# Optimization experiments

Hardware: AMD Instinct MI355X
Metric: run time of the kernel (lower is better)

## Reference

```python
import jax, jax.numpy as jnp
import numpy as np

D = 16          # input_dim (no augmentations)
HID = 256       # hidden_dim
WIN = 64        # window_size
LEN = 1000      # len_noise
INTU = 50       # len_interval_u
B = 512
PAIRS = D * (D - 1) // 2      # 120 depth-2 Lyndon pairs
LOGSIG = D + PAIRS            # 136 logsignature channels


def _static_schedule():
    """Replicates compute_multilevel_logsignature's index logic on static times."""
    tb = np.linspace(0.0, 1.0, LEN)
    tu = tb[::INTU]
    tt = np.linspace(0.0, 1.0, WIN)
    u_indices = np.searchsorted(tb, tu, side='right') - 1
    t_indices = np.searchsorted(tb, tt[1:], side='right') - 1
    u_idx_for_t = np.searchsorted(tu, tt[1:], side='right') - 1
    start_idx = u_indices[np.maximum(u_idx_for_t, 0)]
    # build u_logsigrnn times and the per-step last_h update mask
    qt, last = [], -1
    for iu in u_idx_for_t:
        iu = max(int(iu), 0)
        if iu != last:
            qt.append(tu[iu]); last = iu
    qt.append(tt[-1])
    upd = np.zeros(WIN, dtype=bool)
    for i, t in enumerate(tt):
        if qt and t >= qt[0]:
            qt.pop(0); upd[i] = True
    return tb, t_indices, start_idx, upd


def setup_inputs() -> dict:
    key = jax.random.key(0)
    ks = jax.random.split(key, 6)
    def lin(k, fo, fi):  # kaiming-style fan_in init
        return jax.random.normal(k, (fo, fi), jnp.float32) * np.float32(np.sqrt(2.0 / fi))
    return {
        "z": jax.random.normal(ks[0], (B, LEN, D), jnp.float32),
        "W1": lin(ks[1], HID, HID + LOGSIG), "b1": jnp.zeros((HID,), jnp.float32),
        "W2": lin(ks[2], HID, HID),          "b2": jnp.zeros((HID,), jnp.float32),
        "W3": lin(ks[3], HID, HID),          "b3": jnp.zeros((HID,), jnp.float32),
        "W_lin": lin(ks[4], HID, HID),
    }


def reference(z, W1, b1, W2, b2, W3, b3, W_lin):
    tb, t_idx, s_idx, upd = _static_schedule()
    # Brownian path: z[:,0]=0, z[:,1:] *= sqrt(dt), cumsum
    dt_sqrt = jnp.sqrt(jnp.asarray(np.diff(tb), jnp.float32))          # [LEN-1]
    z = jnp.concatenate([jnp.zeros_like(z[:, :1]), z[:, 1:] * dt_sqrt[None, :, None]], axis=1)
    X = jnp.cumsum(z, axis=1)                                           # [B,LEN,D]
    # depth-2 logsignature with basepoint=0: level1 = X[end]; level2 = Levy area
    iu, ju = np.triu_indices(D, 1)
    Xp, dX = X[:, :-1], X[:, 1:] - X[:, :-1]
    pair = Xp[..., iu] * dX[..., ju] - Xp[..., ju] * dX[..., iu]        # [B,LEN-1,PAIRS]
    C = jnp.concatenate([jnp.zeros_like(pair[:, :1]), jnp.cumsum(pair, axis=1)], axis=1)
    lvl1 = X[:, t_idx]
    levy = 0.5 * (C[:, t_idx] - C[:, s_idx])
    logsig = jnp.concatenate([lvl1, levy], axis=-1)
    logsig = jnp.concatenate([jnp.zeros_like(logsig[:, :1]), logsig], axis=1)  # prepend zeros
    seq = jnp.moveaxis(logsig, 1, 0)

    def mlp(v):  # FeedForwardNN([hid,hid]) + Tanh
        v = jax.nn.relu(v @ W1.T + b1)
        v = jax.nn.relu(v @ W2.T + b2)
        return jnp.tanh(v @ W3.T + b3)

    def step(last_h, xs):
        ls, u = xs
        h = mlp(jnp.concatenate([last_h, ls], axis=-1))
        new_last = jnp.where(u, h, last_h)
        return new_last, h @ W_lin.T

    h0 = jnp.zeros((z.shape[0], HID), z.dtype)  # init_fixed=True
    _, ys = jax.lax.scan(step, h0, (seq, jnp.asarray(upd)))
    return jnp.moveaxis(ys, 0, 1)
```

## Files before the change

### kernel.cpp

```cpp
#include <hip/hip_runtime.h>
#include <hip/hip_bf16.h>
#include <cmath>
#include <cstring>

#define B_SZ   512
#define SLEN   1000
#define DD     16
#define HID    256
#define WIN    64
#define PAIRS  120
#define LSIG   136
#define NWIN   20
#define MAXST  21
#define K1P    416
#define W1FN   (13 * 16 * 64 * 8)
#define WFN    (8 * 16 * 64 * 8)
#define PSTEP  21

using short8 = __attribute__((ext_vector_type(8))) short;
using half8  = __attribute__((ext_vector_type(8))) _Float16;
using f32x4  = __attribute__((ext_vector_type(4))) float;

struct SchedArgs { short snapk[SLEN - 1]; };
struct CombArgs  { unsigned char winofm[WIN]; unsigned char zl[WIN]; };
struct ChainArgs { int nsteps; unsigned char kU[32]; };
struct FuseArgs  { unsigned char sidx[WIN]; };

__device__ __forceinline__ unsigned short f2h(float x) {
  _Float16 h = (_Float16)x;
  return __builtin_bit_cast(unsigned short, h);
}
__device__ __forceinline__ float ftanh(float x) {
  float t = fminf(fmaxf(2.f * x, -30.f), 30.f);
  float e = __expf(t);
  return (e - 1.f) / (e + 1.f);
}

__global__ __launch_bounds__(128) void prep_kernel(
    const float* __restrict__ z,
    const float* __restrict__ W1, const float* __restrict__ W2,
    const float* __restrict__ W3, const float* __restrict__ Wl,
    float* __restrict__ logsig, float* __restrict__ dxwin,
    unsigned short* __restrict__ W1f, unsigned short* __restrict__ W2f,
    unsigned short* __restrict__ W3f, unsigned short* __restrict__ Wlf,
    SchedArgs A)
{
  const int w = blockIdx.x, b = blockIdx.y, tid = threadIdx.x;
  if (w >= NWIN) {
    const int slot = ((w - NWIN) * B_SZ + b) * 128 + tid;
    for (int e = slot; e < W1FN + 3 * WFN; e += 3 * B_SZ * 128) {
      if (e < W1FN) {
        int f = e;
        int j = f & 7, l15 = (f >> 3) & 15, lq = (f >> 7) & 3, nsub = (f >> 9) & 15, kk = f >> 13;
        int row = nsub * 16 + l15, col = kk * 32 + lq * 8 + j;
        float v = (col < HID + LSIG) ? W1[(size_t)row * (HID + LSIG) + col] : 0.f;
        W1f[f] = f2h(v);
      } else {
        int e2 = e - W1FN;
        int which = e2 >> 16, f = e2 & 65535;
        int j = f & 7, l15 = (f >> 3) & 15, lq = (f >> 7) & 3, nsub = (f >> 9) & 15, kk = (f >> 13) & 7;
        int row = nsub * 16 + l15, col = kk * 32 + lq * 8 + j;
        const float* src = which == 0 ? W2 : which == 1 ? W3 : Wl;
        unsigned short* dst = which == 0 ? W2f : which == 1 ? W3f : Wlf;
        dst[f] = f2h(src[(size_t)row * HID + col]);
      }
    }
    return;
  }
  __shared__ float zs[50][16];
  const int ns = (w == NWIN - 1) ? 49 : 50;
  const float* src = z + ((size_t)b * SLEN + 50 * w + 1) * DD;
  const double s999 = 1.0 / (double)(SLEN - 1);
  for (int c = tid; c < ns * 4; c += 128) {
    float4 v = ((const float4*)src)[c];
    int t = 50 * w + (c >> 2);
    double a = (t + 1 == SLEN - 1) ? 1.0 : (double)(t + 1) * s999;
    float s = sqrtf((float)(a - (double)t * s999));
    v.x *= s; v.y *= s; v.z *= s; v.w *= s;
    ((float4*)&zs[0][0])[c] = v;
  }
  int pi = 0, pj = 0;
  if (tid < PAIRS) { int rem = tid, i = 0; while (rem >= DD - 1 - i) { rem -= DD - 1 - i; ++i; } pi = i; pj = i + 1 + rem; }
  __syncthreads();
  float Yi = 0.f, Yj = 0.f, LL = 0.f, Yd = 0.f;
  const int base_t = 50 * w;
  for (int u = 0; u < ns; ++u) {
    const float di = zs[u][pi], dj = zs[u][pj];
    LL = fmaf(Yi, dj, LL); LL = fmaf(-Yj, di, LL);
    Yi += di; Yj += dj;
    if (tid < DD) Yd += zs[u][tid];
    const int m = A.snapk[base_t + u];
    if (m) {
      float* dst = logsig + ((size_t)b * WIN + m) * LSIG;
      if (tid < DD)    dst[tid]      = Yd;
      if (tid < PAIRS) dst[DD + tid] = LL;
    }
  }
  if (tid < DD) dxwin[((size_t)b * NWIN + w) * DD + tid] = Yd;
}

__global__ __launch_bounds__(128) void comb_kernel(
    float* __restrict__ logsig, const float* __restrict__ dxwin, CombArgs A)
{
  const int m = blockIdx.x, b = blockIdx.y, tid = threadIdx.x;
  float* row = logsig + ((size_t)b * WIN + m) * LSIG;
  if (m == 0) {
    if (tid < LSIG) row[tid] = 0.f;
    if (tid + 128 < LSIG) row[tid + 128] = 0.f;
    return;
  }
  __shared__ float Xs[DD], Yt[DD];
  const int w = A.winofm[m];
  if (tid < DD) {
    float acc = 0.f;
    for (int ww = 0; ww < w; ++ww) acc += dxwin[((size_t)b * NWIN + ww) * DD + tid];
    float y = row[tid];
    Xs[tid] = acc; Yt[tid] = y;
    row[tid] = acc + y;
  }
  __syncthreads();
  if (tid < PAIRS) {
    int rem = tid, i = 0; while (rem >= DD - 1 - i) { rem -= DD - 1 - i; ++i; }
    const int pi = i, pj = i + 1 + rem;
    float ll = row[DD + tid];
    row[DD + tid] = A.zl[m] ? 0.f : 0.5f * (ll + Xs[pi] * Yt[pj] - Xs[pj] * Yt[pi]);
  }
}

__global__ __launch_bounds__(256) void psig_kernel(
    const float* __restrict__ logsig, const unsigned short* __restrict__ W1f,
    const float* __restrict__ b1, float* __restrict__ partial, ChainArgs A)
{
  __shared__ __align__(16) unsigned short As[5 * 4 * 16 * 8];
  const int g = blockIdx.x, m = blockIdx.y, tid = threadIdx.x;
  const int lane = tid & 63, w = tid >> 6;
  const int l15 = lane & 15, lq = lane >> 4;
  const int k = A.kU[m];
  for (int idx = tid; idx < 16 * 160; idx += 256) {
    int row = idx / 160, c = idx - row * 160;
    float v = (c < LSIG) ? logsig[(((size_t)(g * 16 + row)) * WIN + k) * LSIG + c] : 0.f;
    As[(((c >> 5) * 4 + ((c >> 3) & 3)) * 16 + row) * 8 + (c & 7)] = f2h(v);
  }
  __syncthreads();
  f32x4 acc[4] = {{0.f,0.f,0.f,0.f},{0.f,0.f,0.f,0.f},{0.f,0.f,0.f,0.f},{0.f,0.f,0.f,0.f}};
#pragma unroll
  for (int kt = 0; kt < 5; ++kt) {
    half8 af = *(const half8*)&As[((kt * 4 + lq) * 16 + l15) * 8];
#pragma unroll
    for (int t = 0; t < 4; ++t) {
      half8 bf = *(const half8*)(W1f + ((size_t)((8 + kt) * 16 + w * 4 + t) * 64 + lane) * 8);
      acc[t] = __builtin_amdgcn_mfma_f32_16x16x32_f16(af, bf, acc[t], 0, 0, 0);
    }
  }
#pragma unroll
  for (int t = 0; t < 4; ++t) {
    int col = w * 64 + t * 16 + l15;
    float bb = b1[col];
    f32x4 r = acc[t];
    r[0] += bb; r[1] += bb; r[2] += bb; r[3] += bb;
    *(f32x4*)&partial[(((size_t)g * PSTEP + m) * HID + col) * 16 + lq * 4] = r;
  }
}

__global__ __attribute__((amdgpu_flat_work_group_size(512, 512)))
__attribute__((amdgpu_waves_per_eu(2, 2)))
void chain_kernel(
    const float* __restrict__ partial,
    const unsigned short* __restrict__ W1f, const unsigned short* __restrict__ W2f,
    const unsigned short* __restrict__ W3f,
    const float* __restrict__ b2, const float* __restrict__ b3,
    unsigned short* __restrict__ statesb, ChainArgs A)
{
  __shared__ __align__(16) unsigned short A0s[32 * 16 * 8];
  __shared__ __align__(16) unsigned short A1s[32 * 16 * 8];
  __shared__ __align__(16) unsigned short A2s[32 * 16 * 8];
  const int tid = threadIdx.x, g = blockIdx.x;
  const int lane = tid & 63, w = tid >> 6;
  const int l15 = lane & 15, lq = lane >> 4;

  for (int c = tid; c < 32 * 16 * 8; c += 512) A0s[c] = 0;
  for (int c = tid; c < 16 * HID; c += 512) {
    int r = c >> 8, col = c & 255;
    statesb[((size_t)(g * 16 + r) * MAXST + 0) * HID + col] = 0;
  }

  half8 W1r[16], W2r[16], W3r[16];
#pragma unroll
  for (int kk = 0; kk < 8; ++kk)
#pragma unroll
    for (int nt = 0; nt < 2; ++nt) {
      W1r[kk * 2 + nt] = *(const half8*)(W1f + ((size_t)(kk * 16 + w * 2 + nt) * 64 + lane) * 8);
      W2r[kk * 2 + nt] = *(const half8*)(W2f + ((size_t)(kk * 16 + w * 2 + nt) * 64 + lane) * 8);
      W3r[kk * 2 + nt] = *(const half8*)(W3f + ((size_t)(kk * 16 + w * 2 + nt) * 64 + lane) * 8);
    }

  float bias2[2], bias3[2];
#pragma unroll
  for (int nt = 0; nt < 2; ++nt) {
    int col = (w * 2 + nt) * 16 + l15;
    bias2[nt] = b2[col]; bias3[nt] = b3[col];
  }

  const float* pbase = partial + ((size_t)g * PSTEP) * HID * 16;
  int poff[2];
#pragma unroll
  for (int nt = 0; nt < 2; ++nt) {
    int col = w * 32 + nt * 16 + l15;
    poff[nt] = col * 16 + lq * 4;
  }
  f32x4 pf[2];
  pf[0] = *(const f32x4*)(pbase + poff[0]);
  pf[1] = *(const f32x4*)(pbase + poff[1]);

  unsigned short hv[2][4];
  __syncthreads();

  for (int m = 0; m < A.nsteps; ++m) {
    if (m > 0) {
#pragma unroll
      for (int nt = 0; nt < 2; ++nt)
#pragma unroll
        for (int r4 = 0; r4 < 4; ++r4) {
          int row = lq * 4 + r4, col = w * 32 + nt * 16 + l15;
          statesb[((size_t)(g * 16 + row) * MAXST + m) * HID + col] = hv[nt][r4];
        }
    }
    {
      f32x4 acc[2][2];
      acc[0][0] = pf[0]; acc[0][1] = pf[1];
      acc[1][0] = (f32x4){0.f,0.f,0.f,0.f}; acc[1][1] = (f32x4){0.f,0.f,0.f,0.f};
      if (m + 1 < A.nsteps) {
        const float* pp = pbase + (size_t)(m + 1) * HID * 16;
        pf[0] = *(const f32x4*)(pp + poff[0]);
        pf[1] = *(const f32x4*)(pp + poff[1]);
      }
#pragma unroll
      for (int kk = 0; kk < 8; ++kk) {
        half8 af = *(const half8*)&A0s[((kk * 4 + lq) * 16 + l15) * 8];
        acc[kk & 1][0] = __builtin_amdgcn_mfma_f32_16x16x32_f16(af, W1r[kk * 2    ], acc[kk & 1][0], 0, 0, 0);
        acc[kk & 1][1] = __builtin_amdgcn_mfma_f32_16x16x32_f16(af, W1r[kk * 2 + 1], acc[kk & 1][1], 0, 0, 0);
      }
#pragma unroll
      for (int nt = 0; nt < 2; ++nt) {
        f32x4 s = acc[0][nt] + acc[1][nt];
        int col = w * 32 + nt * 16 + l15;
        int base = ((col >> 3) * 16) * 8 + (col & 7);
#pragma unroll
        for (int r4 = 0; r4 < 4; ++r4)
          A1s[base + (lq * 4 + r4) * 8] = f2h(fmaxf(s[r4], 0.f));
      }
    }
    __syncthreads();
    {
      f32x4 acc[2][2] = {{{0.f,0.f,0.f,0.f},{0.f,0.f,0.f,0.f}},{{0.f,0.f,0.f,0.f},{0.f,0.f,0.f,0.f}}};
#pragma unroll
      for (int kk = 0; kk < 8; ++kk) {
        half8 af = *(const half8*)&A1s[((kk * 4 + lq) * 16 + l15) * 8];
        acc[kk & 1][0] = __builtin_amdgcn_mfma_f32_16x16x32_f16(af, W2r[kk * 2    ], acc[kk & 1][0], 0, 0, 0);
        acc[kk & 1][1] = __builtin_amdgcn_mfma_f32_16x16x32_f16(af, W2r[kk * 2 + 1], acc[kk & 1][1], 0, 0, 0);
      }
#pragma unroll
      for (int nt = 0; nt < 2; ++nt) {
        f32x4 s = acc[0][nt] + acc[1][nt];
        int col = w * 32 + nt * 16 + l15;
        int base = ((col >> 3) * 16) * 8 + (col & 7);
#pragma unroll
        for (int r4 = 0; r4 < 4; ++r4)
          A2s[base + (lq * 4 + r4) * 8] = f2h(fmaxf(s[r4] + bias2[nt], 0.f));
      }
    }
    __syncthreads();
    {
      f32x4 acc[2][2] = {{{0.f,0.f,0.f,0.f},{0.f,0.f,0.f,0.f}},{{0.f,0.f,0.f,0.f},{0.f,0.f,0.f,0.f}}};
#pragma unroll
      for (int kk = 0; kk < 8; ++kk) {
        half8 af = *(const half8*)&A2s[((kk * 4 + lq) * 16 + l15) * 8];
        acc[kk & 1][0] = __builtin_amdgcn_mfma_f32_16x16x32_f16(af, W3r[kk * 2    ], acc[kk & 1][0], 0, 0, 0);
        acc[kk & 1][1] = __builtin_amdgcn_mfma_f32_16x16x32_f16(af, W3r[kk * 2 + 1], acc[kk & 1][1], 0, 0, 0);
      }
#pragma unroll
      for (int nt = 0; nt < 2; ++nt) {
        f32x4 s = acc[0][nt] + acc[1][nt];
        int col = w * 32 + nt * 16 + l15;
        int base = ((col >> 3) * 16) * 8 + (col & 7);
#pragma unroll
        for (int r4 = 0; r4 < 4; ++r4) {
          float tv = ftanh(s[r4] + bias3[nt]);
          unsigned short hvv = f2h(tv);
          hv[nt][r4] = hvv;
          A0s[base + (lq * 4 + r4) * 8] = hvv;
        }
      }
    }
    __syncthreads();
  }
  {
    const int m = A.nsteps;
#pragma unroll
    for (int nt = 0; nt < 2; ++nt)
#pragma unroll
      for (int r4 = 0; r4 < 4; ++r4) {
        int row = lq * 4 + r4, col = w * 32 + nt * 16 + l15;
        statesb[((size_t)(g * 16 + row) * MAXST + m) * HID + col] = hv[nt][r4];
      }
  }
}

__global__ __launch_bounds__(256, 1) void fused_kernel(
    const unsigned short* __restrict__ statesb, const float* __restrict__ logsig,
    const unsigned short* __restrict__ W1f, const unsigned short* __restrict__ W2f,
    const unsigned short* __restrict__ W3f, const unsigned short* __restrict__ Wlf,
    const float* __restrict__ b1, const float* __restrict__ b2, const float* __restrict__ b3,
    float* __restrict__ out, FuseArgs F)
{
  __shared__ __align__(16) unsigned short act1[32 * 128 * 8];
  __shared__ __align__(16) unsigned short act2[32 * 128 * 8];
  __shared__ __align__(16) unsigned short atile[2][4 * 128 * 8];
  const int tid = threadIdx.x, band = blockIdx.x;
  const int lane = tid & 63, w = tid >> 6;
  const int l15 = lane & 15, lq = lane >> 4;

  float bias1[4], bias2[4], bias3[4];
#pragma unroll
  for (int t = 0; t < 4; ++t) {
    int col = w * 64 + t * 16 + l15;
    bias1[t] = b1[col]; bias2[t] = b2[col]; bias3[t] = b3[col];
  }

  f32x4 acc[8][4];
#pragma unroll
  for (int a = 0; a < 8; ++a)
#pragma unroll
    for (int t = 0; t < 4; ++t) acc[a][t] = (f32x4){0.f, 0.f, 0.f, 0.f};

  short8 pk[2];
  auto loadA = [&](int kk, short8* p) {
#pragma unroll
    for (int i = 0; i < 2; ++i) {
      int c = tid + 256 * i;
      int r = c >> 2, cc = (c & 3) * 8;
      int col = kk * 32 + cc;
      int bA = band * 2 + (r >> 6), ks = r & 63;
      if (col < HID) {
        p[i] = *(const short8*)(statesb + ((size_t)bA * MAXST + F.sidx[ks]) * HID + col);
      } else {
        const float* sp = logsig + ((size_t)bA * WIN + ks) * LSIG + (col - HID);
        float4 v0 = ((const float4*)sp)[0];
        float4 v1 = ((const float4*)sp)[1];
        short8 q;
        q[0] = (short)f2h(v0.x); q[1] = (short)f2h(v0.y); q[2] = (short)f2h(v0.z); q[3] = (short)f2h(v0.w);
        q[4] = (short)f2h(v1.x); q[5] = (short)f2h(v1.y); q[6] = (short)f2h(v1.z); q[7] = (short)f2h(v1.w);
        p[i] = q;
      }
    }
  };
  loadA(0, pk);
  for (int kk = 0; kk < 13; ++kk) {
    unsigned short* buf = atile[kk & 1];
#pragma unroll
    for (int i = 0; i < 2; ++i) {
      int c = tid + 256 * i;
      int r = c >> 2, ch = c & 3;
      *(short8*)&buf[(ch * 128 + r) * 8] = pk[i];
    }
    __syncthreads();
    if (kk + 1 < 13) loadA(kk + 1, pk);
    half8 bfr[4];
#pragma unroll
    for (int t = 0; t < 4; ++t)
      bfr[t] = *(const half8*)(W1f + ((size_t)(kk * 16 + w * 4 + t) * 64 + lane) * 8);
#pragma unroll
    for (int a = 0; a < 8; ++a) {
      half8 af = *(const half8*)&buf[(lq * 128 + a * 16 + l15) * 8];
#pragma unroll
      for (int t = 0; t < 4; ++t)
        acc[a][t] = __builtin_amdgcn_mfma_f32_16x16x32_f16(af, bfr[t], acc[a][t], 0, 0, 0);
    }
    __syncthreads();
  }
#pragma unroll
  for (int a = 0; a < 8; ++a)
#pragma unroll
    for (int t = 0; t < 4; ++t) {
      int col = w * 64 + t * 16 + l15;
      int base = ((col >> 3) * 128) * 8 + (col & 7);
#pragma unroll
      for (int r4 = 0; r4 < 4; ++r4) {
        int row = a * 16 + lq * 4 + r4;
        act1[base + row * 8] = f2h(fmaxf(acc[a][t][r4] + bias1[t], 0.f));
      }
    }
  __syncthreads();

  auto layer = [&](const unsigned short* inb, const unsigned short* Wf) {
#pragma unroll
    for (int a = 0; a < 8; ++a)
#pragma unroll
      for (int t = 0; t < 4; ++t) acc[a][t] = (f32x4){0.f, 0.f, 0.f, 0.f};
    for (int kk = 0; kk < 8; ++kk) {
      half8 bfr[4];
#pragma unroll
      for (int t = 0; t < 4; ++t)
        bfr[t] = *(const half8*)(Wf + ((size_t)(kk * 16 + w * 4 + t) * 64 + lane) * 8);
#pragma unroll
      for (int a = 0; a < 8; ++a) {
        half8 af = *(const half8*)&inb[((kk * 4 + lq) * 128 + a * 16 + l15) * 8];
#pragma unroll
        for (int t = 0; t < 4; ++t)
          acc[a][t] = __builtin_amdgcn_mfma_f32_16x16x32_f16(af, bfr[t], acc[a][t], 0, 0, 0);
      }
    }
  };

  layer(act1, W2f);
#pragma unroll
  for (int a = 0; a < 8; ++a)
#pragma unroll
    for (int t = 0; t < 4; ++t) {
      int col = w * 64 + t * 16 + l15;
      int base = ((col >> 3) * 128) * 8 + (col & 7);
#pragma unroll
      for (int r4 = 0; r4 < 4; ++r4) {
        int row = a * 16 + lq * 4 + r4;
        act2[base + row * 8] = f2h(fmaxf(acc[a][t][r4] + bias2[t], 0.f));
      }
    }
  __syncthreads();

  layer(act2, W3f);
#pragma unroll
  for (int a = 0; a < 8; ++a)
#pragma unroll
    for (int t = 0; t < 4; ++t) {
      int col = w * 64 + t * 16 + l15;
      int base = ((col >> 3) * 128) * 8 + (col & 7);
#pragma unroll
      for (int r4 = 0; r4 < 4; ++r4) {
        int row = a * 16 + lq * 4 + r4;
        act1[base + row * 8] = f2h(ftanh(acc[a][t][r4] + bias3[t]));
      }
    }
  __syncthreads();

  layer(act1, Wlf);
#pragma unroll
  for (int a = 0; a < 8; ++a)
#pragma unroll
    for (int t = 0; t < 4; ++t) {
      int col = w * 64 + t * 16 + l15;
#pragma unroll
      for (int r4 = 0; r4 < 4; ++r4) {
        int row = a * 16 + lq * 4 + r4;
        out[((size_t)(band * 128 + row)) * HID + col] = acc[a][t][r4];
      }
    }
}

static void build_sched(SchedArgs& P, CombArgs& CB, ChainArgs& CH, FuseArgs& FU) {
  double tb[SLEN], tt[WIN], tu[NWIN];
  const double s999 = 1.0 / (double)(SLEN - 1);
  const double s63  = 1.0 / (double)(WIN - 1);
  for (int i = 0; i < SLEN; ++i) tb[i] = (double)i * s999;
  tb[SLEN - 1] = 1.0;
  for (int k = 0; k < WIN; ++k) tt[k] = (double)k * s63;
  tt[WIN - 1] = 1.0;
  for (int j = 0; j < NWIN; ++j) tu[j] = tb[50 * j];

  int t_idx[WIN - 1], u_for_t[WIN - 1];
  for (int k = 1; k < WIN; ++k) {
    int ii = 0;
    for (int q = 0; q < SLEN; ++q) if (tb[q] <= tt[k]) ii = q;
    t_idx[k - 1] = ii;
    int jj = 0;
    for (int q = 0; q < NWIN; ++q) if (tu[q] <= tt[k]) jj = q;
    u_for_t[k - 1] = jj;
  }
  for (int t = 0; t < SLEN - 1; ++t) P.snapk[t] = 0;
  for (int m = 1; m < WIN; ++m) P.snapk[t_idx[m - 1] - 1] = (short)m;

  for (int m = 0; m < WIN; ++m) { CB.winofm[m] = 0; CB.zl[m] = 0; }
  for (int m = 1; m < WIN; ++m) {
    int p = t_idx[m - 1];
    CB.winofm[m] = (unsigned char)((p - 1) / 50);
    CB.zl[m] = (p % 50 == 0) ? 1 : 0;
  }

  double qt[32]; int nq = 0, last = -1;
  for (int m = 0; m < WIN - 1; ++m) {
    const int iu = u_for_t[m];
    if (iu != last) { qt[nq++] = tu[iu]; last = iu; }
  }
  qt[nq++] = tt[WIN - 1];
  int upd[WIN]; int qh = 0;
  for (int i = 0; i < WIN; ++i) {
    upd[i] = 0;
    if (qh < nq && tt[i] >= qt[qh]) { qh++; upd[i] = 1; }
  }
  int nU = 0;
  for (int k = 0; k < WIN; ++k) if (upd[k]) { if (nU < 32) CH.kU[nU] = (unsigned char)k; ++nU; }
  int cnt = 0;
  for (int k = 0; k < WIN; ++k) { FU.sidx[k] = (unsigned char)cnt; if (upd[k]) ++cnt; }
  CH.nsteps = FU.sidx[WIN - 1];
}

extern "C" void kernel_launch(void* const* d_in, const int* in_sizes, int n_in,
                              void* d_out, int out_size, void* d_ws, size_t ws_size,
                              hipStream_t stream) {
  const float* z  = (const float*)d_in[0];
  const float* W1 = (const float*)d_in[1];
  const float* b1 = (const float*)d_in[2];
  const float* W2 = (const float*)d_in[3];
  const float* b2 = (const float*)d_in[4];
  const float* W3 = (const float*)d_in[5];
  const float* b3 = (const float*)d_in[6];
  const float* Wl = (const float*)d_in[7];

  char* ws = (char*)d_ws;
  float* logsig = (float*)(ws);
  size_t o = (size_t)B_SZ * WIN * LSIG * 4;
  float* dxwin            = (float*)(ws + o); o += (size_t)B_SZ * NWIN * DD * 4;
  unsigned short* statesb = (unsigned short*)(ws + o); o += (size_t)B_SZ * MAXST * HID * 2;
  unsigned short* W1f     = (unsigned short*)(ws + o); o += (size_t)W1FN * 2;
  unsigned short* W2f     = (unsigned short*)(ws + o); o += (size_t)WFN * 2;
  unsigned short* W3f     = (unsigned short*)(ws + o); o += (size_t)WFN * 2;
  unsigned short* Wlf     = (unsigned short*)(ws + o); o += (size_t)WFN * 2;
  float* partial          = (float*)(ws + o); o += (size_t)32 * PSTEP * HID * 16 * 4;

  SchedArgs P; CombArgs CB; ChainArgs CH; FuseArgs FU;
  build_sched(P, CB, CH, FU);

  prep_kernel<<<dim3(NWIN + 3, B_SZ), 128, 0, stream>>>(
      z, W1, W2, W3, Wl, logsig, dxwin, W1f, W2f, W3f, Wlf, P);
  comb_kernel<<<dim3(WIN, B_SZ), 128, 0, stream>>>(logsig, dxwin, CB);
  psig_kernel<<<dim3(32, CH.nsteps), 256, 0, stream>>>(logsig, W1f, b1, partial, CH);
  chain_kernel<<<32, 512, 0, stream>>>(partial, W1f, W2f, W3f, b2, b3, statesb, CH);
  fused_kernel<<<256, 256, 0, stream>>>(statesb, logsig, W1f, W2f, W3f, Wlf,
                                        b1, b2, b3, (float*)d_out, FU);
}
```

Baseline: 248.5 us.

## Fuse logsig combine with partial W1 projection and transpose MFMA operands for vector stores

Merges the combine kernel and the logsignature-to-hidden projection kernel into one kernel. Each block handles 16 batch rows for one window step, finalises their logsignature rows and immediately runs the MFMA projection for update steps, which removes one launch and a logsig reload. All MFMA calls swap their A/B operands so each lane holds four consecutive columns. Activations, states and outputs can then be written with vectorised 4-wide stores and biases loaded as f32x4. The partial buffer layout changes to row-major per step to match, and one barrier in the fused layer-1 loop is dropped.

After: 230.5 us. 7.3% less time.

```diff
diff --git a/kernel.cpp b/kernel.cpp
--- a/kernel.cpp
+++ b/kernel.cpp
@@ -17,12 +17,13 @@
 #define WFN    (8 * 16 * 64 * 8)
 #define PSTEP  21
 
-using short8 = __attribute__((ext_vector_type(8))) short;
-using half8  = __attribute__((ext_vector_type(8))) _Float16;
-using f32x4  = __attribute__((ext_vector_type(4))) float;
+using short8  = __attribute__((ext_vector_type(8))) short;
+using short4v = __attribute__((ext_vector_type(4))) short;
+using half8   = __attribute__((ext_vector_type(8))) _Float16;
+using f32x4   = __attribute__((ext_vector_type(4))) float;
 
 struct SchedArgs { short snapk[SLEN - 1]; };
-struct CombArgs  { unsigned char winofm[WIN]; unsigned char zl[WIN]; };
+struct CombPArgs { unsigned char winofm[WIN]; unsigned char zl[WIN]; unsigned char sstep[WIN]; };
 struct ChainArgs { int nsteps; unsigned char kU[32]; };
 struct FuseArgs  { unsigned char sidx[WIN]; };
 
@@ -99,66 +100,60 @@
   if (tid < DD) dxwin[((size_t)b * NWIN + w) * DD + tid] = Yd;
 }
 
-__global__ __launch_bounds__(128) void comb_kernel(
-    float* __restrict__ logsig, const float* __restrict__ dxwin, CombArgs A)
+__global__ __launch_bounds__(256) void combp_kernel(
+    float* __restrict__ logsig, const float* __restrict__ dxwin,
+    const unsigned short* __restrict__ W1f, const float* __restrict__ b1,
+    float* __restrict__ partial, CombPArgs A)
 {
-  const int m = blockIdx.x, b = blockIdx.y, tid = threadIdx.x;
-  float* row = logsig + ((size_t)b * WIN + m) * LSIG;
-  if (m == 0) {
-    if (tid < LSIG) row[tid] = 0.f;
-    if (tid + 128 < LSIG) row[tid + 128] = 0.f;
-    return;
-  }
-  __shared__ float Xs[DD], Yt[DD];
-  const int w = A.winofm[m];
-  if (tid < DD) {
+  __shared__ float Xs[16][16], Yt[16][16];
+  __shared__ __align__(16) unsigned short As[20 * 16 * 8];
+  const int k = blockIdx.x, g = blockIdx.y, tid = threadIdx.x;
+  const int w = A.winofm[k], zl = A.zl[k], ss = A.sstep[k];
+  for (int c = tid; c < 3 * 16 * 8; c += 256) As[17 * 16 * 8 + c] = 0;
+  {
+    const int bi = tid >> 4, col = tid & 15;
+    const size_t b = (size_t)(g * 16 + bi);
     float acc = 0.f;
-    for (int ww = 0; ww < w; ++ww) acc += dxwin[((size_t)b * NWIN + ww) * DD + tid];
-    float y = row[tid];
-    Xs[tid] = acc; Yt[tid] = y;
-    row[tid] = acc + y;
-  }
-  __syncthreads();
-  if (tid < PAIRS) {
-    int rem = tid, i = 0; while (rem >= DD - 1 - i) { rem -= DD - 1 - i; ++i; }
+    for (int ww = 0; ww < w; ++ww) acc += dxwin[(b * NWIN + ww) * DD + col];
+    float y = (k == 0) ? 0.f : logsig[(b * WIN + k) * LSIG + col];
+    float fin = (k == 0) ? 0.f : acc + y;
+    Xs[bi][col] = acc; Yt[bi][col] = y;
+    logsig[(b * WIN + k) * LSIG + col] = fin;
+    As[((col >> 3) * 16 + bi) * 8 + (col & 7)] = f2h(fin);
+  }
+  __syncthreads();
+  for (int idx = tid; idx < 16 * PAIRS; idx += 256) {
+    const int bi = idx / PAIRS, p = idx - bi * PAIRS;
+    int rem = p, i = 0; while (rem >= DD - 1 - i) { rem -= DD - 1 - i; ++i; }
     const int pi = i, pj = i + 1 + rem;
-    float ll = row[DD + tid];
-    row[DD + tid] = A.zl[m] ? 0.f : 0.5f * (ll + Xs[pi] * Yt[pj] - Xs[pj] * Yt[pi]);
-  }
-}
-
-__global__ __launch_bounds__(256) void psig_kernel(
-    const float* __restrict__ logsig, const unsigned short* __restrict__ W1f,
-    const float* __restrict__ b1, float* __restrict__ partial, ChainArgs A)
-{
-  __shared__ __align__(16) unsigned short As[5 * 4 * 16 * 8];
-  const int g = blockIdx.x, m = blockIdx.y, tid = threadIdx.x;
-  const int lane = tid & 63, w = tid >> 6;
+    const size_t b = (size_t)(g * 16 + bi);
+    float ll = (k == 0) ? 0.f : logsig[(b * WIN + k) * LSIG + DD + p];
+    float fin = (k == 0 || zl) ? 0.f
+              : 0.5f * (ll + Xs[bi][pi] * Yt[bi][pj] - Xs[bi][pj] * Yt[bi][pi]);
+    logsig[(b * WIN + k) * LSIG + DD + p] = fin;
+    const int c = DD + p;
+    As[((c >> 3) * 16 + bi) * 8 + (c & 7)] = f2h(fin);
+  }
+  if (ss == 255) return;
+  __syncthreads();
+  const int lane = tid & 63, wv = tid >> 6;
   const int l15 = lane & 15, lq = lane >> 4;
-  const int k = A.kU[m];
-  for (int idx = tid; idx < 16 * 160; idx += 256) {
-    int row = idx / 160, c = idx - row * 160;
-    float v = (c < LSIG) ? logsig[(((size_t)(g * 16 + row)) * WIN + k) * LSIG + c] : 0.f;
-    As[(((c >> 5) * 4 + ((c >> 3) & 3)) * 16 + row) * 8 + (c & 7)] = f2h(v);
-  }
-  __syncthreads();
-  f32x4 acc[4] = {{0.f,0.f,0.f,0.f},{0.f,0.f,0.f,0.f},{0.f,0.f,0.f,0.f},{0.f,0.f,0.f,0.f}};
+  f32x4 acc4[4] = {{0,0,0,0},{0,0,0,0},{0,0,0,0},{0,0,0,0}};
 #pragma unroll
   for (int kt = 0; kt < 5; ++kt) {
     half8 af = *(const half8*)&As[((kt * 4 + lq) * 16 + l15) * 8];
 #pragma unroll
     for (int t = 0; t < 4; ++t) {
-      half8 bf = *(const half8*)(W1f + ((size_t)((8 + kt) * 16 + w * 4 + t) * 64 + lane) * 8);
-      acc[t] = __builtin_amdgcn_mfma_f32_16x16x32_f16(af, bf, acc[t], 0, 0, 0);
+      half8 bfW = *(const half8*)(W1f + ((size_t)((8 + kt) * 16 + wv * 4 + t) * 64 + lane) * 8);
+      acc4[t] = __builtin_amdgcn_mfma_f32_16x16x32_f16(bfW, af, acc4[t], 0, 0, 0);
     }
   }
 #pragma unroll
   for (int t = 0; t < 4; ++t) {
-    int col = w * 64 + t * 16 + l15;
-    float bb = b1[col];
-    f32x4 r = acc[t];
-    r[0] += bb; r[1] += bb; r[2] += bb; r[3] += bb;
-    *(f32x4*)&partial[(((size_t)g * PSTEP + m) * HID + col) * 16 + lq * 4] = r;
+    const int col0 = wv * 64 + t * 16 + lq * 4;
+    f32x4 bb = *(const f32x4*)(b1 + col0);
+    f32x4 r = acc4[t] + bb;
+    *(f32x4*)&partial[(((size_t)g * PSTEP + ss) * 16 + l15) * HID + col0] = r;
   }
 }
 
@@ -194,60 +189,54 @@
       W3r[kk * 2 + nt] = *(const half8*)(W3f + ((size_t)(kk * 16 + w * 2 + nt) * 64 + lane) * 8);
     }
 
-  float bias2[2], bias3[2];
+  int colb[2];
+  f32x4 bias2v[2], bias3v[2];
 #pragma unroll
   for (int nt = 0; nt < 2; ++nt) {
-    int col = (w * 2 + nt) * 16 + l15;
-    bias2[nt] = b2[col]; bias3[nt] = b3[col];
-  }
-
-  const float* pbase = partial + ((size_t)g * PSTEP) * HID * 16;
+    colb[nt] = w * 32 + nt * 16 + lq * 4;
+    bias2v[nt] = *(const f32x4*)(b2 + colb[nt]);
+    bias3v[nt] = *(const f32x4*)(b3 + colb[nt]);
+  }
+
+  const float* pbase = partial + (size_t)g * PSTEP * 16 * HID;
   int poff[2];
 #pragma unroll
-  for (int nt = 0; nt < 2; ++nt) {
-    int col = w * 32 + nt * 16 + l15;
-    poff[nt] = col * 16 + lq * 4;
-  }
+  for (int nt = 0; nt < 2; ++nt) poff[nt] = l15 * HID + colb[nt];
   f32x4 pf[2];
   pf[0] = *(const f32x4*)(pbase + poff[0]);
   pf[1] = *(const f32x4*)(pbase + poff[1]);
 
-  unsigned short hv[2][4];
+  short4v hv4[2];
   __syncthreads();
 
   for (int m = 0; m < A.nsteps; ++m) {
     if (m > 0) {
 #pragma unroll
       for (int nt = 0; nt < 2; ++nt)
-#pragma unroll
-        for (int r4 = 0; r4 < 4; ++r4) {
-          int row = lq * 4 + r4, col = w * 32 + nt * 16 + l15;
-          statesb[((size_t)(g * 16 + row) * MAXST + m) * HID + col] = hv[nt][r4];
-        }
+        *(short4v*)&statesb[((size_t)(g * 16 + l15) * MAXST + m) * HID + colb[nt]] = hv4[nt];
     }
     {
       f32x4 acc[2][2];
       acc[0][0] = pf[0]; acc[0][1] = pf[1];
       acc[1][0] = (f32x4){0.f,0.f,0.f,0.f}; acc[1][1] = (f32x4){0.f,0.f,0.f,0.f};
       if (m + 1 < A.nsteps) {
-        const float* pp = pbase + (size_t)(m + 1) * HID * 16;
+        const float* pp = pbase + (size_t)(m + 1) * 16 * HID;
         pf[0] = *(const f32x4*)(pp + poff[0]);
         pf[1] = *(const f32x4*)(pp + poff[1]);
       }
 #pragma unroll
       for (int kk = 0; kk < 8; ++kk) {
         half8 af = *(const half8*)&A0s[((kk * 4 + lq) * 16 + l15) * 8];
-        acc[kk & 1][0] = __builtin_amdgcn_mfma_f32_16x16x32_f16(af, W1r[kk * 2    ], acc[kk & 1][0], 0, 0, 0);
-        acc[kk & 1][1] = __builtin_amdgcn_mfma_f32_16x16x32_f16(af, W1r[kk * 2 + 1], acc[kk & 1][1], 0, 0, 0);
+        acc[kk & 1][0] = __builtin_amdgcn_mfma_f32_16x16x32_f16(W1r[kk * 2    ], af, acc[kk & 1][0], 0, 0, 0);
+        acc[kk & 1][1] = __builtin_amdgcn_mfma_f32_16x16x32_f16(W1r[kk * 2 + 1], af, acc[kk & 1][1], 0, 0, 0);
       }
 #pragma unroll
       for (int nt = 0; nt < 2; ++nt) {
         f32x4 s = acc[0][nt] + acc[1][nt];
-        int col = w * 32 + nt * 16 + l15;
-        int base = ((col >> 3) * 16) * 8 + (col & 7);
-#pragma unroll
-        for (int r4 = 0; r4 < 4; ++r4)
-          A1s[base + (lq * 4 + r4) * 8] = f2h(fmaxf(s[r4], 0.f));
+        short4v h4;
+#pragma unroll
+        for (int r4 = 0; r4 < 4; ++r4) h4[r4] = (short)f2h(fmaxf(s[r4], 0.f));
+        *(short4v*)&A1s[((colb[nt] >> 3) * 16 + l15) * 8 + (colb[nt] & 7)] = h4;
       }
     }
     __syncthreads();
@@ -256,17 +245,16 @@
 #pragma unroll
       for (int kk = 0; kk < 8; ++kk) {
         half8 af = *(const half8*)&A1s[((kk * 4 + lq) * 16 + l15) * 8];
-        acc[kk & 1][0] = __builtin_amdgcn_mfma_f32_16x16x32_f16(af, W2r[kk * 2    ], acc[kk & 1][0], 0, 0, 0);
-        acc[kk & 1][1] = __builtin_amdgcn_mfma_f32_16x16x32_f16(af, W2r[kk * 2 + 1], acc[kk & 1][1], 0, 0, 0);
+        acc[kk & 1][0] = __builtin_amdgcn_mfma_f32_16x16x32_f16(W2r[kk * 2    ], af, acc[kk & 1][0], 0, 0, 0);
+        acc[kk & 1][1] = __builtin_amdgcn_mfma_f32_16x16x32_f16(W2r[kk * 2 + 1], af, acc[kk & 1][1], 0, 0, 0);
       }
 #pragma unroll
       for (int nt = 0; nt < 2; ++nt) {
-        f32x4 s = acc[0][nt] + acc[1][nt];
-        int col = w * 32 + nt * 16 + l15;
-        int base = ((col >> 3) * 16) * 8 + (col & 7);
-#pragma unroll
-        for (int r4 = 0; r4 < 4; ++r4)
-          A2s[base + (lq * 4 + r4) * 8] = f2h(fmaxf(s[r4] + bias2[nt], 0.f));
+        f32x4 s = acc[0][nt] + acc[1][nt] + bias2v[nt];
+        short4v h4;
+#pragma unroll
+        for (int r4 = 0; r4 < 4; ++r4) h4[r4] = (short)f2h(fmaxf(s[r4], 0.f));
+        *(short4v*)&A2s[((colb[nt] >> 3) * 16 + l15) * 8 + (colb[nt] & 7)] = h4;
       }
     }
     __syncthreads();
@@ -275,21 +263,17 @@
 #pragma unroll
       for (int kk = 0; kk < 8; ++kk) {
         half8 af = *(const half8*)&A2s[((kk * 4 + lq) * 16 + l15) * 8];
-        acc[kk & 1][0] = __builtin_amdgcn_mfma_f32_16x16x32_f16(af, W3r[kk * 2    ], acc[kk & 1][0], 0, 0, 0);
-        acc[kk & 1][1] = __builtin_amdgcn_mfma_f32_16x16x32_f16(af, W3r[kk * 2 + 1], acc[kk & 1][1], 0, 0, 0);
+        acc[kk & 1][0] = __builtin_amdgcn_mfma_f32_16x16x32_f16(W3r[kk * 2    ], af, acc[kk & 1][0], 0, 0, 0);
+        acc[kk & 1][1] = __builtin_amdgcn_mfma_f32_16x16x32_f16(W3r[kk * 2 + 1], af, acc[kk & 1][1], 0, 0, 0);
       }
 #pragma unroll
       for (int nt = 0; nt < 2; ++nt) {
-        f32x4 s = acc[0][nt] + acc[1][nt];
-        int col = w * 32 + nt * 16 + l15;
-        int base = ((col >> 3) * 16) * 8 + (col & 7);
-#pragma unroll
-        for (int r4 = 0; r4 < 4; ++r4) {
-          float tv = ftanh(s[r4] + bias3[nt]);
-          unsigned short hvv = f2h(tv);
-          hv[nt][r4] = hvv;
-          A0s[base + (lq * 4 + r4) * 8] = hvv;
-        }
+        f32x4 s = acc[0][nt] + acc[1][nt] + bias3v[nt];
+        short4v h4;
+#pragma unroll
+        for (int r4 = 0; r4 < 4; ++r4) h4[r4] = (short)f2h(ftanh(s[r4]));
+        hv4[nt] = h4;
+        *(short4v*)&A0s[((colb[nt] >> 3) * 16 + l15) * 8 + (colb[nt] & 7)] = h4;
       }
     }
     __syncthreads();
@@ -298,11 +282,7 @@
     const int m = A.nsteps;
 #pragma unroll
     for (int nt = 0; nt < 2; ++nt)
-#pragma unroll
-      for (int r4 = 0; r4 < 4; ++r4) {
-        int row = lq * 4 + r4, col = w * 32 + nt * 16 + l15;
-        statesb[((size_t)(g * 16 + row) * MAXST + m) * HID + col] = hv[nt][r4];
-      }
+      *(short4v*)&statesb[((size_t)(g * 16 + l15) * MAXST + m) * HID + colb[nt]] = hv4[nt];
   }
 }
 
@@ -319,13 +299,6 @@
   const int tid = threadIdx.x, band = blockIdx.x;
   const int lane = tid & 63, w = tid >> 6;
   const int l15 = lane & 15, lq = lane >> 4;
-
-  float bias1[4], bias2[4], bias3[4];
-#pragma unroll
-  for (int t = 0; t < 4; ++t) {
-    int col = w * 64 + t * 16 + l15;
-    bias1[t] = b1[col]; bias2[t] = b2[col]; bias3[t] = b3[col];
-  }
 
   f32x4 acc[8][4];
 #pragma unroll
@@ -356,7 +329,7 @@
   };
   loadA(0, pk);
   for (int kk = 0; kk < 13; ++kk) {
-    unsigned short* buf = atile[kk & 1];
+    unsigned short* buf = &atile[kk & 1][0];
 #pragma unroll
     for (int i = 0; i < 2; ++i) {
       int c = tid + 256 * i;
@@ -374,22 +347,22 @@
       half8 af = *(const half8*)&buf[(lq * 128 + a * 16 + l15) * 8];
 #pragma unroll
       for (int t = 0; t < 4; ++t)
-        acc[a][t] = __builtin_amdgcn_mfma_f32_16x16x32_f16(af, bfr[t], acc[a][t], 0, 0, 0);
-    }
-    __syncthreads();
-  }
-#pragma unroll
-  for (int a = 0; a < 8; ++a)
-#pragma unroll
-    for (int t = 0; t < 4; ++t) {
-      int col = w * 64 + t * 16 + l15;
-      int base = ((col >> 3) * 128) * 8 + (col & 7);
-#pragma unroll
-      for (int r4 = 0; r4 < 4; ++r4) {
-        int row = a * 16 + lq * 4 + r4;
-        act1[base + row * 8] = f2h(fmaxf(acc[a][t][r4] + bias1[t], 0.f));
-      }
-    }
+        acc[a][t] = __builtin_amdgcn_mfma_f32_16x16x32_f16(bfr[t], af, acc[a][t], 0, 0, 0);
+    }
+  }
+#pragma unroll
+  for (int t = 0; t < 4; ++t) {
+    const int col0 = w * 64 + t * 16 + lq * 4;
+    f32x4 bb = *(const f32x4*)(b1 + col0);
+#pragma unroll
+    for (int a = 0; a < 8; ++a) {
+      const int row = a * 16 + l15;
+      short4v h4;
+#pragma unroll
+      for (int r4 = 0; r4 < 4; ++r4) h4[r4] = (short)f2h(fmaxf(acc[a][t][r4] + bb[r4], 0.f));
+      *(short4v*)&act1[((col0 >> 3) * 128 + row) * 8 + (col0 & 7)] = h4;
+    }
+  }
   __syncthreads();
 
   auto layer = [&](const unsigned short* inb, const unsigned short* Wf) {
@@ -407,56 +380,56 @@
         half8 af = *(const half8*)&inb[((kk * 4 + lq) * 128 + a * 16 + l15) * 8];
 #pragma unroll
         for (int t = 0; t < 4; ++t)
-          acc[a][t] = __builtin_amdgcn_mfma_f32_16x16x32_f16(af, bfr[t], acc[a][t], 0, 0, 0);
+          acc[a][t] = __builtin_amdgcn_mfma_f32_16x16x32_f16(bfr[t], af, acc[a][t], 0, 0, 0);
       }
     }
   };
 
   layer(act1, W2f);
 #pragma unroll
-  for (int a = 0; a < 8; ++a)
-#pragma unroll
-    for (int t = 0; t < 4; ++t) {
-      int col = w * 64 + t * 16 + l15;
-      int base = ((col >> 3) * 128) * 8 + (col & 7);
-#pragma unroll
-      for (int r4 = 0; r4 < 4; ++r4) {
-        int row = a * 16 + lq * 4 + r4;
-        act2[base + row * 8] = f2h(fmaxf(acc[a][t][r4] + bias2[t], 0.f));
-      }
-    }
+  for (int t = 0; t < 4; ++t) {
+    const int col0 = w * 64 + t * 16 + lq * 4;
+    f32x4 bb = *(const f32x4*)(b2 + col0);
+#pragma unroll
+    for (int a = 0; a < 8; ++a) {
+      const int row = a * 16 + l15;
+      short4v h4;
+#pragma unroll
+      for (int r4 = 0; r4 < 4; ++r4) h4[r4] = (short)f2h(fmaxf(acc[a][t][r4] + bb[r4], 0.f));
+      *(short4v*)&act2[((col0 >> 3) * 128 + row) * 8 + (col0 & 7)] = h4;
+    }
+  }
   __syncthreads();
 
   layer(act2, W3f);
 #pragma unroll
-  for (int a = 0; a < 8; ++a)
-#pragma unroll
-    for (int t = 0; t < 4; ++t) {
-      int col = w * 64 + t * 16 + l15;
-      int base = ((col >> 3) * 128) * 8 + (col & 7);
-#pragma unroll
-      for (int r4 = 0; r4 < 4; ++r4) {
-        int row = a * 16 + lq * 4 + r4;
-        act1[base + row * 8] = f2h(ftanh(acc[a][t][r4] + bias3[t]));
-      }
-    }
+  for (int t = 0; t < 4; ++t) {
+    const int col0 = w * 64 + t * 16 + lq * 4;
+    f32x4 bb = *(const f32x4*)(b3 + col0);
+#pragma unroll
+    for (int a = 0; a < 8; ++a) {
+      const int row = a * 16 + l15;
+      short4v h4;
+#pragma unroll
+      for (int r4 = 0; r4 < 4; ++r4) h4[r4] = (short)f2h(ftanh(acc[a][t][r4] + bb[r4]));
+      *(short4v*)&act1[((col0 >> 3) * 128 + row) * 8 + (col0 & 7)] = h4;
+    }
+  }
   __syncthreads();
 
   layer(act1, Wlf);
 #pragma unroll
-  for (int a = 0; a < 8; ++a)
-#pragma unroll
-    for (int t = 0; t < 4; ++t) {
-      int col = w * 64 + t * 16 + l15;
-#pragma unroll
-      for (int r4 = 0; r4 < 4; ++r4) {
-        int row = a * 16 + lq * 4 + r4;
-        out[((size_t)(band * 128 + row)) * HID + col] = acc[a][t][r4];
-      }
-    }
-}
-
-static void build_sched(SchedArgs& P, CombArgs& CB, ChainArgs& CH, FuseArgs& FU) {
+  for (int t = 0; t < 4; ++t) {
+    const int col0 = w * 64 + t * 16 + lq * 4;
+#pragma unroll
+    for (int a = 0; a < 8; ++a) {
+      const int row = a * 16 + l15;
+      *(f32x4*)&out[((size_t)(band * 128 + row)) * HID + col0] = acc[a][t];
+    }
+  }
+}
+
+static void build_sched(SchedArgs& P, CombPArgs& CB, ChainArgs& CH, FuseArgs& FU) {
   double tb[SLEN], tt[WIN], tu[NWIN];
   const double s999 = 1.0 / (double)(SLEN - 1);
   const double s63  = 1.0 / (double)(WIN - 1);
@@ -478,7 +451,7 @@
   for (int t = 0; t < SLEN - 1; ++t) P.snapk[t] = 0;
   for (int m = 1; m < WIN; ++m) P.snapk[t_idx[m - 1] - 1] = (short)m;
 
-  for (int m = 0; m < WIN; ++m) { CB.winofm[m] = 0; CB.zl[m] = 0; }
+  for (int m = 0; m < WIN; ++m) { CB.winofm[m] = 0; CB.zl[m] = 0; CB.sstep[m] = 255; }
   for (int m = 1; m < WIN; ++m) {
     int p = t_idx[m - 1];
     CB.winofm[m] = (unsigned char)((p - 1) / 50);
@@ -501,6 +474,8 @@
   int cnt = 0;
   for (int k = 0; k < WIN; ++k) { FU.sidx[k] = (unsigned char)cnt; if (upd[k]) ++cnt; }
   CH.nsteps = FU.sidx[WIN - 1];
+  for (int s = 0; s < nU && s < 32; ++s)
+    if (s < PSTEP) CB.sstep[CH.kU[s]] = (unsigned char)s;
 }
 
 extern "C" void kernel_launch(void* const* d_in, const int* in_sizes, int n_in,
@@ -524,15 +499,14 @@
   unsigned short* W2f     = (unsigned short*)(ws + o); o += (size_t)WFN * 2;
   unsigned short* W3f     = (unsigned short*)(ws + o); o += (size_t)WFN * 2;
   unsigned short* Wlf     = (unsigned short*)(ws + o); o += (size_t)WFN * 2;
-  float* partial          = (float*)(ws + o); o += (size_t)32 * PSTEP * HID * 16 * 4;
-
-  SchedArgs P; CombArgs CB; ChainArgs CH; FuseArgs FU;
+  float* partial          = (float*)(ws + o); o += (size_t)32 * PSTEP * 16 * HID * 4;
+
+  SchedArgs P; CombPArgs CB; ChainArgs CH; FuseArgs FU;
   build_sched(P, CB, CH, FU);
 
   prep_kernel<<<dim3(NWIN + 3, B_SZ), 128, 0, stream>>>(
       z, W1, W2, W3, Wl, logsig, dxwin, W1f, W2f, W3f, Wlf, P);
-  comb_kernel<<<dim3(WIN, B_SZ), 128, 0, stream>>>(logsig, dxwin, CB);
-  psig_kernel<<<dim3(32, CH.nsteps), 256, 0, stream>>>(logsig, W1f, b1, partial, CH);
+  combp_kernel<<<dim3(WIN, 32), 256, 0, stream>>>(logsig, dxwin, W1f, b1, partial, CB);
   chain_kernel<<<32, 512, 0, stream>>>(partial, W1f, W2f, W3f, b2, b3, statesb, CH);
   fused_kernel<<<256, 256, 0, stream>>>(statesb, logsig, W1f, W2f, W3f, Wlf,
                                         b1, b2, b3, (float*)d_out, FU);
```
